# Optimization experiments

Hardware: AMD Instinct MI355X
Metric: run time of the kernel (lower is better)

## Reference

```python
import jax, jax.numpy as jnp
import numpy as np

B, S, D_IN, D_OUT = 4, 2048, 2048, 2048
EPS = 1e-10


def setup_inputs() -> dict:
    key = jax.random.key(0)
    kx, kw, kb = jax.random.split(key, 3)
    x = jax.random.normal(kx, (B, S, D_IN), dtype=jnp.float32)
    weight = jax.random.normal(kw, (D_OUT, D_IN), dtype=jnp.float32) * 0.02
    bias = jax.random.normal(kb, (D_OUT,), dtype=jnp.float32) * 0.02
    return {"x": x, "weight": weight, "bias": bias}


def reference(x, weight, bias):
    # abs-mean scale over the whole weight matrix (scalar)
    scale = jnp.mean(jnp.abs(weight))
    # ternary quantization: round(w/scale) clamped to {-1, 0, 1}
    w_t = jnp.clip(jnp.round(weight / (scale + EPS)), -1.0, 1.0)
    # straight-through estimator: forward uses w_t*scale, grad flows to weight
    w_ste = weight + jax.lax.stop_gradient(w_t * scale - weight)
    # F.linear: x @ w_ste.T + bias
    return jnp.einsum('bsi,oi->bso', x, w_ste) + bias
```

## Files before the change

kernel.cpp:

```cpp
#include <hip/hip_runtime.h>
#include <hip/hip_bf16.h>
#include <stdint.h>

#define M_DIM 8192
#define N_DIM 2048
#define K_DIM 2048
#define NT    (K_DIM / 64)

typedef float f32x4 __attribute__((ext_vector_type(4)));
typedef short bf16x8 __attribute__((ext_vector_type(8)));

typedef const __attribute__((address_space(1))) char* gp_t;
typedef __attribute__((address_space(3))) char* lp_t;

static __device__ __forceinline__ void gload_lds16(const void* g, void* l) {
  __builtin_amdgcn_global_load_lds((gp_t)(uintptr_t)g, (lp_t)(uint32_t)(uintptr_t)l, 16, 0, 0);
}

static __device__ __forceinline__ unsigned short f2bf(float f) {
  unsigned int u = __float_as_uint(f);
  unsigned int r = (u + 0x7FFFu + ((u >> 16) & 1u)) >> 16;
  return (unsigned short)r;
}

__global__ void cvt_x_absum(const float* __restrict__ x, unsigned short* __restrict__ xb,
                            const float* __restrict__ w, float* __restrict__ partials) {
  const int b = blockIdx.x;
  if (b < 16384) {
    int tid = b * 256 + threadIdx.x;
    float4 v = ((const float4*)x)[tid];
    ushort4 o;
    o.x = f2bf(v.x); o.y = f2bf(v.y); o.z = f2bf(v.z); o.w = f2bf(v.w);
    ((ushort4*)xb)[tid] = o;
  } else {
    int tid = (b - 16384) * 256 + threadIdx.x;
    const float4* w4 = (const float4*)w;
    float s = 0.f;
#pragma unroll
    for (int i = 0; i < 4; ++i) {
      float4 v = w4[tid + i * 262144];
      s += fabsf(v.x) + fabsf(v.y) + fabsf(v.z) + fabsf(v.w);
    }
#pragma unroll
    for (int off = 32; off > 0; off >>= 1) s += __shfl_down(s, off, 64);
    __shared__ float ls[4];
    if ((threadIdx.x & 63) == 0) ls[threadIdx.x >> 6] = s;
    __syncthreads();
    if (threadIdx.x == 0) partials[b - 16384] = (ls[0] + ls[1]) + (ls[2] + ls[3]);
  }
}

__global__ void quant_w(const float* __restrict__ w, const float* __restrict__ partials,
                        unsigned short* __restrict__ wt, float* __restrict__ scale_out) {
  __shared__ float ls[4];
  float s = 0.f;
#pragma unroll
  for (int i = 0; i < 4; ++i) s += partials[threadIdx.x + i * 256];
#pragma unroll
  for (int off = 32; off > 0; off >>= 1) s += __shfl_down(s, off, 64);
  if ((threadIdx.x & 63) == 0) ls[threadIdx.x >> 6] = s;
  __syncthreads();
  const float scale = ((ls[0] + ls[1]) + (ls[2] + ls[3])) * (1.0f / 4194304.0f);
  if (blockIdx.x == 0 && threadIdx.x == 0) scale_out[0] = scale;

  const float inv = 1.0f / (scale + 1e-10f);
  int tid = blockIdx.x * 256 + threadIdx.x;
  float4 v = ((const float4*)w)[tid];
  ushort4 o;
  float t;
  t = fminf(1.f, fmaxf(-1.f, rintf(v.x * inv))); o.x = f2bf(t);
  t = fminf(1.f, fmaxf(-1.f, rintf(v.y * inv))); o.y = f2bf(t);
  t = fminf(1.f, fmaxf(-1.f, rintf(v.z * inv))); o.z = f2bf(t);
  t = fminf(1.f, fmaxf(-1.f, rintf(v.w * inv))); o.w = f2bf(t);
  ((ushort4*)wt)[tid] = o;
}


#define VMCNT(n) asm volatile("s_waitcnt vmcnt(" #n ")" ::: "memory")
#define FENCE    asm volatile("" ::: "memory")
#define BARRIER  do { FENCE; __builtin_amdgcn_s_barrier(); FENCE; } while (0)

#define READ_A_TO(base, mh, dst)                                                                \
  do {                                                                                          \
    _Pragma("unroll") for (int i = 0; i < 4; ++i) {                                             \
      dst[i][0] = *(const bf16x8*)((base) + (wr * 128 + (mh) * 64 + i * 16) * 128 + rd0);       \
      dst[i][1] = *(const bf16x8*)((base) + (wr * 128 + (mh) * 64 + i * 16) * 128 + rd1);       \
    }                                                                                           \
  } while (0)

#define READ_B_TO(base, nh, dst)                                                                \
  do {                                                                                          \
    _Pragma("unroll") for (int j = 0; j < 2; ++j) {                                             \
      dst[j][0] = *(const bf16x8*)((base) + (wc * 64 + (nh) * 32 + j * 16) * 128 + rd0);        \
      dst[j][1] = *(const bf16x8*)((base) + (wc * 64 + (nh) * 32 + j * 16) * 128 + rd1);        \
    }                                                                                           \
  } while (0)

#define MFMA_Q(mh, nh, ar, br)                                                                  \
  do {                                                                                          \
    __builtin_amdgcn_s_setprio(1);                                                              \
    _Pragma("unroll") for (int i = 0; i < 4; ++i)                                               \
      _Pragma("unroll") for (int j = 0; j < 2; ++j)                                             \
        acc[(mh) * 4 + i][(nh) * 2 + j] = __builtin_amdgcn_mfma_f32_16x16x32_bf16(              \
            ar[i][0], br[j][0], acc[(mh) * 4 + i][(nh) * 2 + j], 0, 0, 0);                      \
    _Pragma("unroll") for (int i = 0; i < 4; ++i)                                               \
      _Pragma("unroll") for (int j = 0; j < 2; ++j)                                             \
        acc[(mh) * 4 + i][(nh) * 2 + j] = __builtin_amdgcn_mfma_f32_16x16x32_bf16(              \
            ar[i][1], br[j][1], acc[(mh) * 4 + i][(nh) * 2 + j], 0, 0, 0);                      \
    __builtin_amdgcn_s_setprio(0);                                                              \
  } while (0)

#define SA(bufsel, r) gload_lds16(Ag + offA[r] + ktA, ldsb + (bufsel) * 65536 + tid * 16 + (r) * 8192)
#define SB(bufsel, r) gload_lds16(Bg + offB[r] + ktB, ldsb + (bufsel) * 65536 + 32768 + tid * 16 + (r) * 8192)

__global__ void __launch_bounds__(512, 2)
gemm_bt(const unsigned short* __restrict__ A, const unsigned short* __restrict__ Bt,
        const float* __restrict__ bias, const float* __restrict__ scale_p,
        float* __restrict__ out) {
  __shared__ __align__(16) char lds_raw[131072];
  char* ldsb = (char*)lds_raw;

  const int tid = threadIdx.x;
  const int lane = tid & 63;
  const int wid = tid >> 6;
  const int wr = wid >> 2;
  const int wc = wid & 3;
  const int l15 = lane & 15, lhi = lane >> 4;

  const int swzl = (l15 & 7) << 4;
  const int rd0 = l15 * 128 + ((lhi * 16) ^ swzl);
  const int rd1 = l15 * 128 + (((lhi * 16) ^ 64) ^ swzl);

  const int bid = blockIdx.x;
  const int swz = (bid & 7) * 32 + (bid >> 3);
  const int bm = swz >> 3;
  const int bn = swz & 7;
  const int m0 = bm << 8, n0 = bn << 8;

  const int srow = tid >> 3;
  const int scol = (((tid & 7) ^ ((tid >> 3) & 7)) << 4);
  const char* Ag = (const char*)A;
  const char* Bg = (const char*)Bt;
  uint32_t offA[4], offB[4];
#pragma unroll
  for (int r = 0; r < 4; ++r) {
    offA[r] = (uint32_t)(m0 + srow + r * 64) * (K_DIM * 2) + scol;
    offB[r] = (uint32_t)(n0 + srow + r * 64) * (K_DIM * 2) + scol;
  }
  uint32_t ktA = 0, ktB = 0;

  f32x4 acc[8][4];
#pragma unroll
  for (int m = 0; m < 8; ++m)
#pragma unroll
    for (int n = 0; n < 4; ++n) {
      f32x4 z = {0.f, 0.f, 0.f, 0.f};
      acc[m][n] = z;
    }

  SA(0, 0); SA(0, 1); SA(0, 2); SA(0, 3);
  SB(0, 0); SB(0, 1); SB(0, 2); SB(0, 3);
  ktB = 128;
  SB(1, 0); SB(1, 1); SB(1, 2); SB(1, 3);
  ktA = 128; ktB = 256;
  VMCNT(4);
  BARRIER;

  bf16x8 a0[4][2], a1[4][2], b0[2][2], b1[2][2];

  {
    const char* c0A = ldsb;
    const char* c0B = ldsb + 32768;
    READ_A_TO(c0A, 0, a0);
    READ_B_TO(c0B, 0, b0);
  }

  for (int t = 0; t < NT; ++t) {
    const int cb = t & 1;
    const char* curA = ldsb + cb * 65536;
    const char* curB = curA + 32768;
    const char* nxtA = ldsb + (cb ^ 1) * 65536;
    const char* nxtB = nxtA + 32768;

    READ_B_TO(curB, 1, b1);
    if (t < NT - 1) { SA(cb ^ 1, 0); SA(cb ^ 1, 1); }
    MFMA_Q(0, 0, a0, b0);

    READ_A_TO(curA, 1, a1);
    if (t < NT - 1) { SA(cb ^ 1, 2); SA(cb ^ 1, 3); ktA += 128; }
    MFMA_Q(0, 1, a0, b1);

    VMCNT(0);
    BARRIER;

    if (t < NT - 1) READ_A_TO(nxtA, 0, a0);
    if (t < NT - 2) { SB(cb, 0); SB(cb, 1); }
    MFMA_Q(1, 0, a1, b0);
    if (t < NT - 1) READ_B_TO(nxtB, 0, b0);

    if (t < NT - 2) { SB(cb, 2); SB(cb, 3); ktB += 128; }
    MFMA_Q(1, 1, a1, b1);

    BARRIER;
  }

  const float scale = scale_p[0];
#pragma unroll
  for (int n = 0; n < 4; ++n) {
    const int col = n0 + wc * 64 + n * 16 + l15;
    const float bv = bias[col];
#pragma unroll
    for (int m = 0; m < 8; ++m) {
      const int r0 = m0 + wr * 128 + m * 16 + lhi * 4;
      float* op = out + (size_t)r0 * N_DIM + col;
#pragma unroll
      for (int j = 0; j < 4; ++j) op[(size_t)j * N_DIM] = acc[m][n][j] * scale + bv;
    }
  }
}

extern "C" void kernel_launch(void* const* d_in, const int* in_sizes, int n_in,
                              void* d_out, int out_size, void* d_ws, size_t ws_size,
                              hipStream_t stream) {
  (void)in_sizes; (void)n_in; (void)out_size; (void)ws_size;
  const float* x    = (const float*)d_in[0];
  const float* w    = (const float*)d_in[1];
  const float* bias = (const float*)d_in[2];
  float* out = (float*)d_out;

  float* partials = (float*)d_ws;
  float* scale_slot = partials + 1024;
  unsigned short* wt = (unsigned short*)((char*)d_ws + 8192);
  unsigned short* xb = (unsigned short*)((char*)d_ws + 8192 + (size_t)N_DIM * K_DIM * 2);

  cvt_x_absum<<<17408, 256, 0, stream>>>(x, xb, w, partials);
  quant_w<<<4096, 256, 0, stream>>>(w, partials, wt, scale_slot);
  gemm_bt<<<256, 512, 0, stream>>>(xb, wt, bias, scale_slot, out);
}
```

Before: 87.60 us.

## Restructure GEMM main loop to load all LDS fragments upfront and relax vmcnt waits

```diff
diff --git a/kernel.cpp b/kernel.cpp
--- a/kernel.cpp
+++ b/kernel.cpp
@@ -80,19 +80,19 @@
 #define FENCE    asm volatile("" ::: "memory")
 #define BARRIER  do { FENCE; __builtin_amdgcn_s_barrier(); FENCE; } while (0)
 
-#define READ_A_TO(base, mh, dst)                                                                \
+#define READ_A_TO(mh, dst)                                                                      \
   do {                                                                                          \
     _Pragma("unroll") for (int i = 0; i < 4; ++i) {                                             \
-      dst[i][0] = *(const bf16x8*)((base) + (wr * 128 + (mh) * 64 + i * 16) * 128 + rd0);       \
-      dst[i][1] = *(const bf16x8*)((base) + (wr * 128 + (mh) * 64 + i * 16) * 128 + rd1);       \
+      dst[i][0] = *(const bf16x8*)(curA + (wr * 128 + (mh) * 64 + i * 16) * 128 + rd0);         \
+      dst[i][1] = *(const bf16x8*)(curA + (wr * 128 + (mh) * 64 + i * 16) * 128 + rd1);         \
     }                                                                                           \
   } while (0)
 
-#define READ_B_TO(base, nh, dst)                                                                \
+#define READ_B_TO(nh, dst)                                                                      \
   do {                                                                                          \
     _Pragma("unroll") for (int j = 0; j < 2; ++j) {                                             \
-      dst[j][0] = *(const bf16x8*)((base) + (wc * 64 + (nh) * 32 + j * 16) * 128 + rd0);        \
-      dst[j][1] = *(const bf16x8*)((base) + (wc * 64 + (nh) * 32 + j * 16) * 128 + rd1);        \
+      dst[j][0] = *(const bf16x8*)(curB + (wc * 64 + (nh) * 32 + j * 16) * 128 + rd0);          \
+      dst[j][1] = *(const bf16x8*)(curB + (wc * 64 + (nh) * 32 + j * 16) * 128 + rd1);          \
     }                                                                                           \
   } while (0)
 
@@ -168,39 +168,31 @@
 
   bf16x8 a0[4][2], a1[4][2], b0[2][2], b1[2][2];
 
-  {
-    const char* c0A = ldsb;
-    const char* c0B = ldsb + 32768;
-    READ_A_TO(c0A, 0, a0);
-    READ_B_TO(c0B, 0, b0);
-  }
-
   for (int t = 0; t < NT; ++t) {
     const int cb = t & 1;
     const char* curA = ldsb + cb * 65536;
     const char* curB = curA + 32768;
-    const char* nxtA = ldsb + (cb ^ 1) * 65536;
-    const char* nxtB = nxtA + 32768;
-
-    READ_B_TO(curB, 1, b1);
-    if (t < NT - 1) { SA(cb ^ 1, 0); SA(cb ^ 1, 1); }
+
+    READ_A_TO(0, a0);
+    READ_B_TO(0, b0);
+    READ_B_TO(1, b1);
+    READ_A_TO(1, a1);
+    if (t < NT - 1) { SA(cb ^ 1, 0); SA(cb ^ 1, 1); SA(cb ^ 1, 2); SA(cb ^ 1, 3); ktA += 128; }
+
     MFMA_Q(0, 0, a0, b0);
-
-    READ_A_TO(curA, 1, a1);
-    if (t < NT - 1) { SA(cb ^ 1, 2); SA(cb ^ 1, 3); ktA += 128; }
     MFMA_Q(0, 1, a0, b1);
 
-    VMCNT(0);
     BARRIER;
 
-    if (t < NT - 1) READ_A_TO(nxtA, 0, a0);
-    if (t < NT - 2) { SB(cb, 0); SB(cb, 1); }
+    if (t < NT - 2) { SB(cb, 0); SB(cb, 1); SB(cb, 2); SB(cb, 3); ktB += 128; }
     MFMA_Q(1, 0, a1, b0);
-    if (t < NT - 1) READ_B_TO(nxtB, 0, b0);
-
-    if (t < NT - 2) { SB(cb, 2); SB(cb, 3); ktB += 128; }
     MFMA_Q(1, 1, a1, b1);
 
+    if (t < NT - 2) {
+      VMCNT(4);
+    } else {
+      VMCNT(0);
+    }
     BARRIER;
   }
 
```

Measured after the change: 84.60 us. 3.4% less time.

## Restructure K-loop pipeline with partial vmcnt waits and unrolled double buffers

Applied to the files above, without the earlier changes.

```diff
diff --git a/kernel.cpp b/kernel.cpp
--- a/kernel.cpp
+++ b/kernel.cpp
@@ -80,7 +80,7 @@
 #define FENCE    asm volatile("" ::: "memory")
 #define BARRIER  do { FENCE; __builtin_amdgcn_s_barrier(); FENCE; } while (0)
 
-#define READ_A_TO(base, mh, dst)                                                                \
+#define READ_A(base, mh, dst)                                                                   \
   do {                                                                                          \
     _Pragma("unroll") for (int i = 0; i < 4; ++i) {                                             \
       dst[i][0] = *(const bf16x8*)((base) + (wr * 128 + (mh) * 64 + i * 16) * 128 + rd0);       \
@@ -88,7 +88,7 @@
     }                                                                                           \
   } while (0)
 
-#define READ_B_TO(base, nh, dst)                                                                \
+#define READ_B(base, nh, dst)                                                                   \
   do {                                                                                          \
     _Pragma("unroll") for (int j = 0; j < 2; ++j) {                                             \
       dst[j][0] = *(const bf16x8*)((base) + (wc * 64 + (nh) * 32 + j * 16) * 128 + rd0);        \
@@ -113,6 +113,31 @@
 #define SA(bufsel, r) gload_lds16(Ag + offA[r] + ktA, ldsb + (bufsel) * 65536 + tid * 16 + (r) * 8192)
 #define SB(bufsel, r) gload_lds16(Bg + offB[r] + ktB, ldsb + (bufsel) * 65536 + 32768 + tid * 16 + (r) * 8192)
 
+#define TILE_BODY(CURSEL, NXTSEL, t)                                                            \
+  do {                                                                                          \
+    const char* curA = ldsb + (CURSEL) * 65536;                                                 \
+    const char* curB = curA + 32768;                                                            \
+    READ_A(curA, 0, a0);                                                                        \
+    READ_B(curB, 0, b0);                                                                        \
+    if ((t) < NT - 1) { SA(NXTSEL, 0); SA(NXTSEL, 1); }                                         \
+    MFMA_Q(0, 0, a0, b0);                                                                       \
+    READ_B(curB, 1, b1);                                                                        \
+    if ((t) < NT - 1) { SA(NXTSEL, 2); SA(NXTSEL, 3); ktA += 128; }                             \
+    MFMA_Q(0, 1, a0, b1);                                                                       \
+    BARRIER;        \
+    READ_A(curA, 1, a1);                                                                        \
+    if ((t) < NT - 2) { SB(CURSEL, 0); SB(CURSEL, 1); }                                         \
+    MFMA_Q(1, 0, a1, b0);                                                                       \
+    if ((t) < NT - 2) {                                                                         \
+      SB(CURSEL, 2); SB(CURSEL, 3); ktB += 128;                                                 \
+      VMCNT(4);                \
+    } else {                                                                                    \
+      VMCNT(0);                                                                                 \
+    }                                                                                           \
+    MFMA_Q(1, 1, a1, b1);                                                                       \
+    BARRIER;                                  \
+  } while (0)
+
 __global__ void __launch_bounds__(512, 2)
 gemm_bt(const unsigned short* __restrict__ A, const unsigned short* __restrict__ Bt,
         const float* __restrict__ bias, const float* __restrict__ scale_p,
@@ -168,40 +193,10 @@
 
   bf16x8 a0[4][2], a1[4][2], b0[2][2], b1[2][2];
 
-  {
-    const char* c0A = ldsb;
-    const char* c0B = ldsb + 32768;
-    READ_A_TO(c0A, 0, a0);
-    READ_B_TO(c0B, 0, b0);
-  }
-
-  for (int t = 0; t < NT; ++t) {
-    const int cb = t & 1;
-    const char* curA = ldsb + cb * 65536;
-    const char* curB = curA + 32768;
-    const char* nxtA = ldsb + (cb ^ 1) * 65536;
-    const char* nxtB = nxtA + 32768;
-
-    READ_B_TO(curB, 1, b1);
-    if (t < NT - 1) { SA(cb ^ 1, 0); SA(cb ^ 1, 1); }
-    MFMA_Q(0, 0, a0, b0);
-
-    READ_A_TO(curA, 1, a1);
-    if (t < NT - 1) { SA(cb ^ 1, 2); SA(cb ^ 1, 3); ktA += 128; }
-    MFMA_Q(0, 1, a0, b1);
-
-    VMCNT(0);
-    BARRIER;
-
-    if (t < NT - 1) READ_A_TO(nxtA, 0, a0);
-    if (t < NT - 2) { SB(cb, 0); SB(cb, 1); }
-    MFMA_Q(1, 0, a1, b0);
-    if (t < NT - 1) READ_B_TO(nxtB, 0, b0);
-
-    if (t < NT - 2) { SB(cb, 2); SB(cb, 3); ktB += 128; }
-    MFMA_Q(1, 1, a1, b1);
-
-    BARRIER;
+  for (int it = 0; it < NT / 2; ++it) {
+    const int t0 = 2 * it;
+    TILE_BODY(0, 1, t0);
+    TILE_BODY(1, 0, t0 + 1);
   }
 
   const float scale = scale_p[0];
```

Result: faster. 82.94 us, median of 2 (-5.3%).
